# Performance work log

Measured on AMD Instinct MI355X. Metric: run time of the kernel, lower is better.

The kernel has to match this reference:

```python
import jax, jax.numpy as jnp
import numpy as np

N_NODES = 100000
N_EDGES = 1600000
N_GRAPHS = 512
NODE_DIM = 64   # len(node_indices)
GRAPH_DIM = 16  # len(graph_indices) == graph_channels
HIDDEN = 128
OUT = 8


def setup_inputs() -> dict:
    key = jax.random.key(0)
    ks = jax.random.split(key, 12)
    x = jax.random.normal(ks[0], (N_NODES, NODE_DIM + GRAPH_DIM), dtype=jnp.float32)
    edge_index = jax.random.randint(ks[1], (2, N_EDGES), 0, N_NODES, dtype=jnp.int64)
    batch = jnp.sort(jax.random.randint(ks[2], (N_NODES,), 0, N_GRAPHS, dtype=jnp.int64))
    def lin(k, fan_in, fan_out):
        lim = 1.0 / np.sqrt(fan_in)
        return jax.random.uniform(k, (fan_in, fan_out), jnp.float32, -lim, lim)
    return {
        "x": x, "edge_index": edge_index, "batch": batch,
        "W1": lin(ks[3], NODE_DIM, HIDDEN), "b1": jnp.zeros((HIDDEN,), jnp.float32),
        "W2": lin(ks[4], HIDDEN, HIDDEN),   "b2": jnp.zeros((HIDDEN,), jnp.float32),
        "Wm1": lin(ks[5], HIDDEN + GRAPH_DIM, HIDDEN), "bm1": jnp.zeros((HIDDEN,), jnp.float32),
        "Wm2": lin(ks[6], HIDDEN, OUT), "bm2": jnp.zeros((OUT,), jnp.float32),
    }


def _gcn_conv(h_in, src, dst, W, b):
    # PyG GCNConv: h = X W; out = D^{-1/2}(A+I)D^{-1/2} h + b, deg over A+I.
    h = h_in @ W                                        # [N, H]
    deg = jnp.zeros((N_NODES,), h.dtype).at[dst].add(1.0) + 1.0  # +1 self loop
    dinv = jax.lax.rsqrt(deg)                           # [N]
    norm = dinv[src] * dinv[dst]                        # [E]
    out = jnp.zeros_like(h).at[dst].add(norm[:, None] * h[src])
    out = out + (dinv * dinv)[:, None] * h              # self-loop term
    return out + b


def _mean_pool(v, batch):
    cnt = jax.ops.segment_sum(jnp.ones((v.shape[0],), v.dtype), batch, num_segments=N_GRAPHS)
    s = jax.ops.segment_sum(v, batch, num_segments=N_GRAPHS)
    return s / jnp.maximum(cnt, 1.0)[:, None]


def reference(x, edge_index, batch, W1, b1, W2, b2, Wm1, bm1, Wm2, bm2):
    src, dst = edge_index[0], edge_index[1]
    node_t = x[:, :NODE_DIM]                 # node_indices slice
    graph_t = _mean_pool(x[:, NODE_DIM:], batch)  # graph_indices slice, pooled [G, 16]
    h = _gcn_conv(node_t, src, dst, W1, b1)
    h = jax.nn.relu(h)                       # dropout is identity in eval mode
    h = _gcn_conv(h, src, dst, W2, b2)
    g = _mean_pool(h, batch)                 # [G, H]
    g = jnp.concatenate([g, graph_t], axis=1)
    g = jax.nn.relu(g @ Wm1 + bm1)
    return g @ Wm2 + bm2                     # [G, OUT]
```

## Files before the change

### kernel.cpp

```cpp
#include <hip/hip_runtime.h>
#include <hip/hip_bf16.h>

#define N_NODES 100000
#define N_EDGES 1600000
#define N_GRAPHS 512
#define NODE_DIM 64
#define GRAPH_DIM 16
#define HIDDEN 128
#define OUT_DIM 8

#define NBUCKETS 391
#define BIN_CAP 8192
#define EPB 4096

__device__ __forceinline__ float bflo(unsigned u) { return __uint_as_float(u << 16); }
__device__ __forceinline__ float bfhi(unsigned u) { return __uint_as_float(u & 0xffff0000u); }


__global__ __launch_bounds__(256) void k_binplace(const int* __restrict__ src,
                                                  const int* __restrict__ dst,
                                                  int* __restrict__ gcur,
                                                  unsigned* __restrict__ bin) {
    __shared__ int cnt[NBUCKETS];
    __shared__ int base[NBUCKETS];
    int t = threadIdx.x;
    for (int i = t; i < NBUCKETS; i += 256) cnt[i] = 0;
    __syncthreads();
    int e0 = blockIdx.x * EPB;
#pragma unroll
    for (int k = 0; k < EPB / 256; k++) {
        int e = e0 + k * 256 + t;
        if (e < N_EDGES) atomicAdd(&cnt[dst[e] >> 8], 1);
    }
    __syncthreads();
    for (int i = t; i < NBUCKETS; i += 256) {
        int c = cnt[i];
        base[i] = (c > 0) ? atomicAdd(&gcur[i], c) : 0;
        cnt[i] = 0;
    }
    __syncthreads();
#pragma unroll
    for (int k = 0; k < EPB / 256; k++) {
        int e = e0 + k * 256 + t;
        if (e < N_EDGES) {
            int d = dst[e];
            int b = d >> 8;
            int p = atomicAdd(&cnt[b], 1);
            bin[(size_t)b * BIN_CAP + base[b] + p] = ((unsigned)src[e] << 8) | (unsigned)(d & 255);
        }
    }
}


__global__ __launch_bounds__(256) void k_degBf(const int* __restrict__ gcur,
                                               const unsigned* __restrict__ bin,
                                               int* __restrict__ degcnt,
                                               float* __restrict__ dinv,
                                               int* __restrict__ bsum) {
    __shared__ int cnt[256];
    int b = blockIdx.x, t = threadIdx.x;
    cnt[t] = 0;
    __syncthreads();
    int n = gcur[b];
    const unsigned* seg = bin + (size_t)b * BIN_CAP;
    for (int i = t; i < n; i += 256) atomicAdd(&cnt[seg[i] & 255u], 1);
    __syncthreads();
    int c = cnt[t];
    int node = b * 256 + t;
    if (node < N_NODES) {
        degcnt[node] = c;
        dinv[node] = rsqrtf((float)c + 1.0f);
    }
    __syncthreads();
    for (int o = 128; o > 0; o >>= 1) {
        if (t < o) cnt[t] += cnt[t + o];
        __syncthreads();
    }
    if (t == 0) bsum[b] = cnt[0];
}


__global__ __launch_bounds__(512) void k_scanb(const int* __restrict__ bsum,
                                               int* __restrict__ bofs) {
    __shared__ int s[512];
    int t = threadIdx.x;
    int v = (t < NBUCKETS) ? bsum[t] : 0;
    s[t] = v;
    __syncthreads();
    for (int o = 1; o < 512; o <<= 1) {
        int u = (t >= o) ? s[t - o] : 0;
        __syncthreads();
        s[t] += u;
        __syncthreads();
    }
    if (t < NBUCKETS) bofs[t] = s[t] - v;
}


__global__ __launch_bounds__(256) void k_rowfill(const int* __restrict__ degcnt,
                                                 const int* __restrict__ bofs,
                                                 const int* __restrict__ gcur,
                                                 const unsigned* __restrict__ bin,
                                                 const float* __restrict__ dinv,
                                                 int* __restrict__ row_start,
                                                 int2* __restrict__ csre,
                                                 float* __restrict__ gt_sum) {
    __shared__ int sc[256];
    __shared__ int rsl[256];
    __shared__ int cnt[256];
    __shared__ float dl[256];
    int b = blockIdx.x, t = threadIdx.x;
    if (b < 32) gt_sum[b * 256 + t] = 0.0f;
    int node = b * 256 + t;
    int v = (node < N_NODES) ? degcnt[node] : 0;
    sc[t] = v;
    __syncthreads();
    for (int o = 1; o < 256; o <<= 1) {
        int u = (t >= o) ? sc[t - o] : 0;
        __syncthreads();
        sc[t] += u;
        __syncthreads();
    }
    int rs = bofs[b] + sc[t] - v;
    if (node < N_NODES) row_start[node] = rs;
    rsl[t] = rs;
    cnt[t] = 0;
    dl[t] = rsqrtf((float)v + 1.0f);
    __syncthreads();
    int n = gcur[b];
    const unsigned* seg = bin + (size_t)b * BIN_CAP;
    for (int i = t; i < n; i += 256) {
        unsigned e = seg[i];
        int dlidx = (int)(e & 255u);
        int s = (int)(e >> 8);
        int pos = rsl[dlidx] + atomicAdd(&cnt[dlidx], 1);
        csre[pos] = make_int2(s, __float_as_int(dinv[s] * dl[dlidx]));
    }
}


__global__ __launch_bounds__(256) void k_packstat(const float* __restrict__ x,
                                                  const int* __restrict__ batch,
                                                  ushort* __restrict__ xb,
                                                  float* __restrict__ gt_sum) {
    int t = threadIdx.x;
    int i0 = blockIdx.x * 64;
    for (int idx = t; idx < 64 * 32; idx += 256) {
        int node = i0 + (idx >> 5);
        if (node < N_NODES) {
            int c2 = idx & 31;
            float2 v = *(const float2*)&x[(size_t)node * 80 + c2 * 2];
            __hip_bfloat16 lo = __float2bfloat16(v.x);
            __hip_bfloat16 hi = __float2bfloat16(v.y);
            ushort2 pv = make_ushort2(*(ushort*)&lo, *(ushort*)&hi);
            ((ushort2*)xb)[(size_t)node * 32 + c2] = pv;
        }
    }
    int c = t & 15, sub = t >> 4;
    int iend = min(i0 + 64, N_NODES);
    float acc = 0.0f;
    int g = -1;
    for (int i = i0 + sub; i < iend; i += 16) {
        int bi = batch[i];
        if (bi != g) {
            if (g >= 0) atomicAdd(&gt_sum[g * GRAPH_DIM + c], acc);
            acc = 0.0f; g = bi;
        }
        acc += x[(size_t)i * 80 + NODE_DIM + c];
    }
    if (g >= 0) atomicAdd(&gt_sum[g * GRAPH_DIM + c], acc);
}


__global__ __launch_bounds__(256) void k_gather1(const int2* __restrict__ csre,
                                                 const int* __restrict__ row_start,
                                                 const float* __restrict__ dinv,
                                                 const unsigned* __restrict__ xb32,
                                                 float2* __restrict__ z2) {
    int w = threadIdx.x >> 6;
    int half = (threadIdx.x >> 5) & 1;
    int l = threadIdx.x & 31;
    int node = blockIdx.x * 8 + w * 2 + half;
    int rs = row_start[node];
    int re = (node == N_NODES - 1) ? N_EDGES : row_start[node + 1];
    float2 a0 = {0.f, 0.f}, a1 = {0.f, 0.f}, a2 = {0.f, 0.f}, a3 = {0.f, 0.f};
    int k = rs;
    for (; k + 4 <= re; k += 4) {
        int2 e0 = csre[k], e1 = csre[k + 1], e2 = csre[k + 2], e3 = csre[k + 3];
        unsigned u0 = xb32[(size_t)e0.x * 32 + l];
        unsigned u1 = xb32[(size_t)e1.x * 32 + l];
        unsigned u2 = xb32[(size_t)e2.x * 32 + l];
        unsigned u3 = xb32[(size_t)e3.x * 32 + l];
        float w0 = __int_as_float(e0.y), w1 = __int_as_float(e1.y);
        float w2 = __int_as_float(e2.y), w3 = __int_as_float(e3.y);
        a0.x += w0 * bflo(u0); a0.y += w0 * bfhi(u0);
        a1.x += w1 * bflo(u1); a1.y += w1 * bfhi(u1);
        a2.x += w2 * bflo(u2); a2.y += w2 * bfhi(u2);
        a3.x += w3 * bflo(u3); a3.y += w3 * bfhi(u3);
    }
    if (k + 2 <= re) {
        int2 e0 = csre[k], e1 = csre[k + 1];
        unsigned u0 = xb32[(size_t)e0.x * 32 + l];
        unsigned u1 = xb32[(size_t)e1.x * 32 + l];
        float w0 = __int_as_float(e0.y), w1 = __int_as_float(e1.y);
        a0.x += w0 * bflo(u0); a0.y += w0 * bfhi(u0);
        a1.x += w1 * bflo(u1); a1.y += w1 * bfhi(u1);
        k += 2;
    }
    if (k < re) {
        int2 e0 = csre[k];
        unsigned u0 = xb32[(size_t)e0.x * 32 + l];
        float w0 = __int_as_float(e0.y);
        a0.x += w0 * bflo(u0); a0.y += w0 * bfhi(u0);
    }
    float d = dinv[node];
    unsigned us = xb32[(size_t)node * 32 + l];
    float2 r;
    r.x = a0.x + a1.x + a2.x + a3.x + d * d * bflo(us);
    r.y = a0.y + a1.y + a2.y + a3.y + d * d * bfhi(us);
    z2[(size_t)node * 32 + l] = r;
}


__global__ __launch_bounds__(128) void k_gemm64(const float* __restrict__ A,
                                                const float* __restrict__ W,
                                                const float* __restrict__ bias,
                                                ushort* __restrict__ C, int nrows,
                                                float* __restrict__ gsum2) {
    const int TM = 8, K = 64;
    __shared__ float As[TM][K];
    if (blockIdx.x < 512) gsum2[blockIdx.x * 128 + threadIdx.x] = 0.0f;
    int row0 = blockIdx.x * TM;
    int j = threadIdx.x;
    for (int idx = threadIdx.x; idx < TM * K; idx += 128) {
        int m = idx / K, k = idx % K;
        int r = row0 + m;
        As[m][k] = (r < nrows) ? A[(size_t)r * K + k] : 0.0f;
    }
    __syncthreads();
    float acc[TM];
#pragma unroll
    for (int m = 0; m < TM; m++) acc[m] = 0.0f;
    for (int k = 0; k < K; k++) {
        float w = W[k * 128 + j];
#pragma unroll
        for (int m = 0; m < TM; m++) acc[m] += As[m][k] * w;
    }
    float b = bias[j];
#pragma unroll
    for (int m = 0; m < TM; m++) {
        int r = row0 + m;
        if (r < nrows) {
            float v = fmaxf(acc[m] + b, 0.0f);
            __hip_bfloat16 hv = __float2bfloat16(v);
            C[(size_t)r * 128 + j] = *(ushort*)&hv;
        }
    }
}


__global__ __launch_bounds__(256) void k_gather2(const int2* __restrict__ csre,
                                                 const int* __restrict__ row_start,
                                                 const float* __restrict__ dinv,
                                                 const uint2* __restrict__ h2,
                                                 const int* __restrict__ batch,
                                                 float* __restrict__ gsum2) {
    __shared__ float4 red[8][32];
    int w = threadIdx.x >> 6;
    int half = (threadIdx.x >> 5) & 1;
    int l = threadIdx.x & 31;
    int slot = w * 2 + half;
    int node = blockIdx.x * 8 + slot;
    int rs = row_start[node];
    int re = (node == N_NODES - 1) ? N_EDGES : row_start[node + 1];
    float4 a0 = {0,0,0,0}, a1 = {0,0,0,0}, a2 = {0,0,0,0}, a3 = {0,0,0,0};
#define FMA4(acc_, w_, u_) { acc_.x += (w_) * bflo((u_).x); acc_.y += (w_) * bfhi((u_).x); \
                             acc_.z += (w_) * bflo((u_).y); acc_.w += (w_) * bfhi((u_).y); }
    int k = rs;
    for (; k + 4 <= re; k += 4) {
        int2 e0 = csre[k], e1 = csre[k + 1], e2 = csre[k + 2], e3 = csre[k + 3];
        uint2 u0 = h2[(size_t)e0.x * 32 + l];
        uint2 u1 = h2[(size_t)e1.x * 32 + l];
        uint2 u2 = h2[(size_t)e2.x * 32 + l];
        uint2 u3 = h2[(size_t)e3.x * 32 + l];
        float w0 = __int_as_float(e0.y), w1 = __int_as_float(e1.y);
        float w2 = __int_as_float(e2.y), w3 = __int_as_float(e3.y);
        FMA4(a0, w0, u0); FMA4(a1, w1, u1); FMA4(a2, w2, u2); FMA4(a3, w3, u3);
    }
    if (k + 2 <= re) {
        int2 e0 = csre[k], e1 = csre[k + 1];
        uint2 u0 = h2[(size_t)e0.x * 32 + l];
        uint2 u1 = h2[(size_t)e1.x * 32 + l];
        float w0 = __int_as_float(e0.y), w1 = __int_as_float(e1.y);
        FMA4(a0, w0, u0); FMA4(a1, w1, u1);
        k += 2;
    }
    if (k < re) {
        int2 e0 = csre[k];
        uint2 u0 = h2[(size_t)e0.x * 32 + l];
        float w0 = __int_as_float(e0.y);
        FMA4(a0, w0, u0);
    }
#undef FMA4
    float d = dinv[node];
    float dd = d * d;
    uint2 us = h2[(size_t)node * 32 + l];
    float4 r;
    r.x = a0.x + a1.x + a2.x + a3.x + dd * bflo(us.x);
    r.y = a0.y + a1.y + a2.y + a3.y + dd * bfhi(us.x);
    r.z = a0.z + a1.z + a2.z + a3.z + dd * bflo(us.y);
    r.w = a0.w + a1.w + a2.w + a3.w + dd * bfhi(us.y);
    red[slot][l] = r;
    __syncthreads();
    int base8 = blockIdx.x * 8;
    int g0 = batch[base8];
    int g7 = batch[base8 + 7];
    if (g0 == g7) {
        if (threadIdx.x < 32) {
            float4 s = {0,0,0,0};
#pragma unroll
            for (int q = 0; q < 8; q++) {
                float4 v = red[q][threadIdx.x];
                s.x += v.x; s.y += v.y; s.z += v.z; s.w += v.w;
            }
            atomicAdd(&gsum2[g0 * 128 + threadIdx.x * 4 + 0], s.x);
            atomicAdd(&gsum2[g0 * 128 + threadIdx.x * 4 + 1], s.y);
            atomicAdd(&gsum2[g0 * 128 + threadIdx.x * 4 + 2], s.z);
            atomicAdd(&gsum2[g0 * 128 + threadIdx.x * 4 + 3], s.w);
        }
    } else {
        int g = batch[node];
        atomicAdd(&gsum2[g * 128 + l * 4 + 0], r.x);
        atomicAdd(&gsum2[g * 128 + l * 4 + 1], r.y);
        atomicAdd(&gsum2[g * 128 + l * 4 + 2], r.z);
        atomicAdd(&gsum2[g * 128 + l * 4 + 3], r.w);
    }
}


__global__ __launch_bounds__(128) void k_mlp(const float* __restrict__ gsum2,
                                             const float* __restrict__ gt_sum,
                                             const int* __restrict__ batch,
                                             const float* __restrict__ W2,
                                             const float* __restrict__ b2,
                                             const float* __restrict__ Wm1,
                                             const float* __restrict__ bm1,
                                             const float* __restrict__ Wm2,
                                             const float* __restrict__ bm2,
                                             float* __restrict__ out) {
    __shared__ float srow[HIDDEN];
    __shared__ float g144[HIDDEN + GRAPH_DIM];
    __shared__ float sm[HIDDEN];
    __shared__ int cnt_sh;
    int b = blockIdx.x;
    int j = threadIdx.x;
    float raw = gsum2[b * 128 + j];
    float gtraw = (j < GRAPH_DIM) ? gt_sum[b * GRAPH_DIM + j] : 0.0f;
    if (j == 0) {
        int lo = 0, hi = N_NODES;
        while (lo < hi) { int m = (lo + hi) >> 1; if (batch[m] < b) lo = m + 1; else hi = m; }
        int a = lo;
        lo = 0; hi = N_NODES;
        while (lo < hi) { int m = (lo + hi) >> 1; if (batch[m] < b + 1) lo = m + 1; else hi = m; }
        cnt_sh = lo - a;
    }
    __syncthreads();
    float inv = 1.0f / fmaxf((float)cnt_sh, 1.0f);
    srow[j] = raw * inv;
    if (j < GRAPH_DIM) g144[128 + j] = gtraw * inv;
    __syncthreads();
    float z = b2[j];
    for (int k = 0; k < 128; k++) z += srow[k] * W2[k * 128 + j];
    g144[j] = z;
    __syncthreads();
    float acc = bm1[j];
    for (int k = 0; k < HIDDEN + GRAPH_DIM; k++) acc += g144[k] * Wm1[k * 128 + j];
    sm[j] = fmaxf(acc, 0.0f);
    __syncthreads();
    if (j < OUT_DIM) {
        float o = bm2[j];
        for (int k = 0; k < 128; k++) o += sm[k] * Wm2[k * OUT_DIM + j];
        out[b * OUT_DIM + j] = o;
    }
}

extern "C" void kernel_launch(void* const* d_in, const int* in_sizes, int n_in,
                              void* d_out, int out_size, void* d_ws, size_t ws_size,
                              hipStream_t stream) {
    const float* x    = (const float*)d_in[0];
    const int*   edge = (const int*)d_in[1];
    const int*   src  = edge;
    const int*   dst  = edge + N_EDGES;
    const int*   batch= (const int*)d_in[2];
    const float* W1   = (const float*)d_in[3];
    const float* b1   = (const float*)d_in[4];
    const float* W2   = (const float*)d_in[5];
    const float* b2   = (const float*)d_in[6];
    const float* Wm1  = (const float*)d_in[7];
    const float* bm1  = (const float*)d_in[8];
    const float* Wm2  = (const float*)d_in[9];
    const float* bm2  = (const float*)d_in[10];
    float* out = (float*)d_out;

    char* ws = (char*)d_ws;
    char* p = ws;
    unsigned* bin   = (unsigned*)p;  p += (size_t)NBUCKETS * BIN_CAP * 4;
    int2*  csre     = (int2*)p;      p += (size_t)N_EDGES * 8;
    float* A        = (float*)p;     p += (size_t)N_NODES * 64 * 4;
    ushort* h1b     = (ushort*)p;    p += (size_t)N_NODES * 128 * 2;
    ushort* xb      = (ushort*)p;    p += (size_t)N_NODES * 64 * 2;
    int*   degcnt   = (int*)p;       p += (size_t)NBUCKETS * 256 * 4;
    int*   row_start= (int*)p;       p += (size_t)N_NODES * 4;
    float* dinv     = (float*)p;     p += (size_t)N_NODES * 4;
    int*   gcur     = (int*)p;       p += (size_t)NBUCKETS * 4;
    int*   bsum     = (int*)p;       p += 512 * 4;
    int*   bofs     = (int*)p;       p += 512 * 4;
    float* gt_sum   = (float*)p;     p += (size_t)N_GRAPHS * GRAPH_DIM * 4;
    float* gsum2    = (float*)p;     p += (size_t)N_GRAPHS * 128 * 4;

    hipMemsetAsync(gcur, 0, (size_t)NBUCKETS * 4, stream);

    k_binplace<<<(N_EDGES + EPB - 1) / EPB, 256, 0, stream>>>(src, dst, gcur, bin);
    k_degBf<<<NBUCKETS, 256, 0, stream>>>(gcur, bin, degcnt, dinv, bsum);
    k_scanb<<<1, 512, 0, stream>>>(bsum, bofs);
    k_rowfill<<<NBUCKETS, 256, 0, stream>>>(degcnt, bofs, gcur, bin, dinv, row_start, csre, gt_sum);

    k_packstat<<<(N_NODES + 63) / 64, 256, 0, stream>>>(x, batch, xb, gt_sum);

    k_gather1<<<N_NODES / 8, 256, 0, stream>>>(csre, row_start, dinv, (const unsigned*)xb, (float2*)A);
    k_gemm64<<<(N_NODES + 7) / 8, 128, 0, stream>>>(A, W1, b1, h1b, N_NODES, gsum2);

    k_gather2<<<N_NODES / 8, 256, 0, stream>>>(csre, row_start, dinv,
                                               (const uint2*)h1b, batch, gsum2);

    k_mlp<<<N_GRAPHS, 128, 0, stream>>>(gsum2, gt_sum, batch, W2, b2, Wm1, bm1, Wm2, bm2, out);
}
```

Before: 258.1 us.

## Fuse layer-1 gather with the 64x128 GEMM and use a full wave per node

Merges the first aggregation kernel with the dense W1 transform, so aggregated rows stay in shared memory and are never written to or read back from the fp32 intermediate buffer. Both gather kernels now give each node a full 64-lane wave, with the two halves taking alternate edges and combining via a cross-half shuffle, and blocks grow to 512 threads. This removes a launch and an intermediate round trip and raises per-node memory parallelism. In exchange there is more shuffle and select work per edge, and the fused GEMM runs on only 8 rows per block, each thread re-reading W1 from global memory.

```diff
diff --git a/kernel.cpp b/kernel.cpp
--- a/kernel.cpp
+++ b/kernel.cpp
@@ -172,168 +172,175 @@
 }
 
 
-__global__ __launch_bounds__(256) void k_gather1(const int2* __restrict__ csre,
-                                                 const int* __restrict__ row_start,
-                                                 const float* __restrict__ dinv,
-                                                 const unsigned* __restrict__ xb32,
-                                                 float2* __restrict__ z2) {
-    int w = threadIdx.x >> 6;
-    int half = (threadIdx.x >> 5) & 1;
-    int l = threadIdx.x & 31;
-    int node = blockIdx.x * 8 + w * 2 + half;
+__global__ __launch_bounds__(512) void k_conv1(const int2* __restrict__ csre,
+                                               const int* __restrict__ row_start,
+                                               const float* __restrict__ dinv,
+                                               const unsigned* __restrict__ xb32,
+                                               const float* __restrict__ W,
+                                               const float* __restrict__ bias,
+                                               ushort* __restrict__ C,
+                                               float* __restrict__ gsum2) {
+    __shared__ float zs[8][64];
+    int t = threadIdx.x;
+    if (blockIdx.x < 128) gsum2[blockIdx.x * 512 + t] = 0.0f;
+    int wv = t >> 6;
+    int lane = t & 63;
+    int half = lane >> 5;
+    int l5 = lane & 31;
+    int node = blockIdx.x * 8 + wv;
     int rs = row_start[node];
     int re = (node == N_NODES - 1) ? N_EDGES : row_start[node + 1];
-    float2 a0 = {0.f, 0.f}, a1 = {0.f, 0.f}, a2 = {0.f, 0.f}, a3 = {0.f, 0.f};
+    float2 a0 = {0.f,0.f}, a1 = {0.f,0.f}, a2 = {0.f,0.f}, a3 = {0.f,0.f};
     int k = rs;
-    for (; k + 4 <= re; k += 4) {
-        int2 e0 = csre[k], e1 = csre[k + 1], e2 = csre[k + 2], e3 = csre[k + 3];
-        unsigned u0 = xb32[(size_t)e0.x * 32 + l];
-        unsigned u1 = xb32[(size_t)e1.x * 32 + l];
-        unsigned u2 = xb32[(size_t)e2.x * 32 + l];
-        unsigned u3 = xb32[(size_t)e3.x * 32 + l];
-        float w0 = __int_as_float(e0.y), w1 = __int_as_float(e1.y);
-        float w2 = __int_as_float(e2.y), w3 = __int_as_float(e3.y);
+    for (; k + 8 <= re; k += 8) {
+        int2 e0 = csre[k],     e1 = csre[k + 1], e2 = csre[k + 2], e3 = csre[k + 3];
+        int2 e4 = csre[k + 4], e5 = csre[k + 5], e6 = csre[k + 6], e7 = csre[k + 7];
+        int   r0 = half ? e1.x : e0.x;  float w0 = __int_as_float(half ? e1.y : e0.y);
+        int   r1 = half ? e3.x : e2.x;  float w1 = __int_as_float(half ? e3.y : e2.y);
+        int   r2 = half ? e5.x : e4.x;  float w2 = __int_as_float(half ? e5.y : e4.y);
+        int   r3 = half ? e7.x : e6.x;  float w3 = __int_as_float(half ? e7.y : e6.y);
+        unsigned u0 = xb32[(size_t)r0 * 32 + l5];
+        unsigned u1 = xb32[(size_t)r1 * 32 + l5];
+        unsigned u2 = xb32[(size_t)r2 * 32 + l5];
+        unsigned u3 = xb32[(size_t)r3 * 32 + l5];
         a0.x += w0 * bflo(u0); a0.y += w0 * bfhi(u0);
         a1.x += w1 * bflo(u1); a1.y += w1 * bfhi(u1);
         a2.x += w2 * bflo(u2); a2.y += w2 * bfhi(u2);
         a3.x += w3 * bflo(u3); a3.y += w3 * bfhi(u3);
     }
-    if (k + 2 <= re) {
+    for (; k + 2 <= re; k += 2) {
         int2 e0 = csre[k], e1 = csre[k + 1];
-        unsigned u0 = xb32[(size_t)e0.x * 32 + l];
-        unsigned u1 = xb32[(size_t)e1.x * 32 + l];
-        float w0 = __int_as_float(e0.y), w1 = __int_as_float(e1.y);
+        int r0 = half ? e1.x : e0.x;  float w0 = __int_as_float(half ? e1.y : e0.y);
+        unsigned u0 = xb32[(size_t)r0 * 32 + l5];
         a0.x += w0 * bflo(u0); a0.y += w0 * bfhi(u0);
-        a1.x += w1 * bflo(u1); a1.y += w1 * bfhi(u1);
-        k += 2;
     }
     if (k < re) {
         int2 e0 = csre[k];
-        unsigned u0 = xb32[(size_t)e0.x * 32 + l];
-        float w0 = __int_as_float(e0.y);
+        float w0 = half ? 0.0f : __int_as_float(e0.y);
+        unsigned u0 = xb32[(size_t)e0.x * 32 + l5];
         a0.x += w0 * bflo(u0); a0.y += w0 * bfhi(u0);
     }
-    float d = dinv[node];
-    unsigned us = xb32[(size_t)node * 32 + l];
-    float2 r;
-    r.x = a0.x + a1.x + a2.x + a3.x + d * d * bflo(us);
-    r.y = a0.y + a1.y + a2.y + a3.y + d * d * bfhi(us);
-    z2[(size_t)node * 32 + l] = r;
-}
-
-
-__global__ __launch_bounds__(128) void k_gemm64(const float* __restrict__ A,
-                                                const float* __restrict__ W,
-                                                const float* __restrict__ bias,
-                                                ushort* __restrict__ C, int nrows,
-                                                float* __restrict__ gsum2) {
-    const int TM = 8, K = 64;
-    __shared__ float As[TM][K];
-    if (blockIdx.x < 512) gsum2[blockIdx.x * 128 + threadIdx.x] = 0.0f;
-    int row0 = blockIdx.x * TM;
-    int j = threadIdx.x;
-    for (int idx = threadIdx.x; idx < TM * K; idx += 128) {
-        int m = idx / K, k = idx % K;
-        int r = row0 + m;
-        As[m][k] = (r < nrows) ? A[(size_t)r * K + k] : 0.0f;
-    }
-    __syncthreads();
-    float acc[TM];
-#pragma unroll
-    for (int m = 0; m < TM; m++) acc[m] = 0.0f;
-    for (int k = 0; k < K; k++) {
-        float w = W[k * 128 + j];
-#pragma unroll
-        for (int m = 0; m < TM; m++) acc[m] += As[m][k] * w;
-    }
-    float b = bias[j];
-#pragma unroll
-    for (int m = 0; m < TM; m++) {
-        int r = row0 + m;
-        if (r < nrows) {
-            float v = fmaxf(acc[m] + b, 0.0f);
-            __hip_bfloat16 hv = __float2bfloat16(v);
-            C[(size_t)r * 128 + j] = *(ushort*)&hv;
+    float sx = a0.x + a1.x + a2.x + a3.x;
+    float sy = a0.y + a1.y + a2.y + a3.y;
+    sx += __shfl_xor(sx, 32);
+    sy += __shfl_xor(sy, 32);
+    if (half == 0) {
+        float d = dinv[node];
+        float dd = d * d;
+        unsigned us = xb32[(size_t)node * 32 + l5];
+        zs[wv][2 * l5]     = sx + dd * bflo(us);
+        zs[wv][2 * l5 + 1] = sy + dd * bfhi(us);
+    }
+    __syncthreads();
+    {
+        int j = t & 127;
+        int g = t >> 7;
+        float acc0 = 0.f, acc1 = 0.f;
+        for (int kk = 0; kk < 64; kk++) {
+            float wk = W[kk * 128 + j];
+            acc0 += zs[2 * g][kk] * wk;
+            acc1 += zs[2 * g + 1][kk] * wk;
         }
-    }
-}
-
-
-__global__ __launch_bounds__(256) void k_gather2(const int2* __restrict__ csre,
+        float b = bias[j];
+        size_t row0 = (size_t)blockIdx.x * 8 + 2 * g;
+        float v0 = fmaxf(acc0 + b, 0.0f);
+        float v1 = fmaxf(acc1 + b, 0.0f);
+        __hip_bfloat16 h0 = __float2bfloat16(v0);
+        __hip_bfloat16 h1 = __float2bfloat16(v1);
+        C[row0 * 128 + j]       = *(ushort*)&h0;
+        C[(row0 + 1) * 128 + j] = *(ushort*)&h1;
+    }
+}
+
+
+__global__ __launch_bounds__(512) void k_gather2(const int2* __restrict__ csre,
                                                  const int* __restrict__ row_start,
                                                  const float* __restrict__ dinv,
                                                  const uint2* __restrict__ h2,
                                                  const int* __restrict__ batch,
                                                  float* __restrict__ gsum2) {
     __shared__ float4 red[8][32];
-    int w = threadIdx.x >> 6;
-    int half = (threadIdx.x >> 5) & 1;
-    int l = threadIdx.x & 31;
-    int slot = w * 2 + half;
-    int node = blockIdx.x * 8 + slot;
+    int t = threadIdx.x;
+    int wv = t >> 6;
+    int lane = t & 63;
+    int half = lane >> 5;
+    int l5 = lane & 31;
+    int node = blockIdx.x * 8 + wv;
     int rs = row_start[node];
     int re = (node == N_NODES - 1) ? N_EDGES : row_start[node + 1];
     float4 a0 = {0,0,0,0}, a1 = {0,0,0,0}, a2 = {0,0,0,0}, a3 = {0,0,0,0};
 #define FMA4(acc_, w_, u_) { acc_.x += (w_) * bflo((u_).x); acc_.y += (w_) * bfhi((u_).x); \
                              acc_.z += (w_) * bflo((u_).y); acc_.w += (w_) * bfhi((u_).y); }
     int k = rs;
-    for (; k + 4 <= re; k += 4) {
-        int2 e0 = csre[k], e1 = csre[k + 1], e2 = csre[k + 2], e3 = csre[k + 3];
-        uint2 u0 = h2[(size_t)e0.x * 32 + l];
-        uint2 u1 = h2[(size_t)e1.x * 32 + l];
-        uint2 u2 = h2[(size_t)e2.x * 32 + l];
-        uint2 u3 = h2[(size_t)e3.x * 32 + l];
-        float w0 = __int_as_float(e0.y), w1 = __int_as_float(e1.y);
-        float w2 = __int_as_float(e2.y), w3 = __int_as_float(e3.y);
+    for (; k + 8 <= re; k += 8) {
+        int2 e0 = csre[k],     e1 = csre[k + 1], e2 = csre[k + 2], e3 = csre[k + 3];
+        int2 e4 = csre[k + 4], e5 = csre[k + 5], e6 = csre[k + 6], e7 = csre[k + 7];
+        int   r0 = half ? e1.x : e0.x;  float w0 = __int_as_float(half ? e1.y : e0.y);
+        int   r1 = half ? e3.x : e2.x;  float w1 = __int_as_float(half ? e3.y : e2.y);
+        int   r2 = half ? e5.x : e4.x;  float w2 = __int_as_float(half ? e5.y : e4.y);
+        int   r3 = half ? e7.x : e6.x;  float w3 = __int_as_float(half ? e7.y : e6.y);
+        uint2 u0 = h2[(size_t)r0 * 32 + l5];
+        uint2 u1 = h2[(size_t)r1 * 32 + l5];
+        uint2 u2 = h2[(size_t)r2 * 32 + l5];
+        uint2 u3 = h2[(size_t)r3 * 32 + l5];
         FMA4(a0, w0, u0); FMA4(a1, w1, u1); FMA4(a2, w2, u2); FMA4(a3, w3, u3);
     }
-    if (k + 2 <= re) {
+    for (; k + 2 <= re; k += 2) {
         int2 e0 = csre[k], e1 = csre[k + 1];
-        uint2 u0 = h2[(size_t)e0.x * 32 + l];
-        uint2 u1 = h2[(size_t)e1.x * 32 + l];
-        float w0 = __int_as_float(e0.y), w1 = __int_as_float(e1.y);
-        FMA4(a0, w0, u0); FMA4(a1, w1, u1);
-        k += 2;
+        int r0 = half ? e1.x : e0.x;  float w0 = __int_as_float(half ? e1.y : e0.y);
+        uint2 u0 = h2[(size_t)r0 * 32 + l5];
+        FMA4(a0, w0, u0);
     }
     if (k < re) {
         int2 e0 = csre[k];
-        uint2 u0 = h2[(size_t)e0.x * 32 + l];
-        float w0 = __int_as_float(e0.y);
+        float w0 = half ? 0.0f : __int_as_float(e0.y);
+        uint2 u0 = h2[(size_t)e0.x * 32 + l5];
         FMA4(a0, w0, u0);
     }
 #undef FMA4
-    float d = dinv[node];
-    float dd = d * d;
-    uint2 us = h2[(size_t)node * 32 + l];
+    float4 s;
+    s.x = a0.x + a1.x + a2.x + a3.x;
+    s.y = a0.y + a1.y + a2.y + a3.y;
+    s.z = a0.z + a1.z + a2.z + a3.z;
+    s.w = a0.w + a1.w + a2.w + a3.w;
+    s.x += __shfl_xor(s.x, 32);
+    s.y += __shfl_xor(s.y, 32);
+    s.z += __shfl_xor(s.z, 32);
+    s.w += __shfl_xor(s.w, 32);
     float4 r;
-    r.x = a0.x + a1.x + a2.x + a3.x + dd * bflo(us.x);
-    r.y = a0.y + a1.y + a2.y + a3.y + dd * bfhi(us.x);
-    r.z = a0.z + a1.z + a2.z + a3.z + dd * bflo(us.y);
-    r.w = a0.w + a1.w + a2.w + a3.w + dd * bfhi(us.y);
-    red[slot][l] = r;
+    if (half == 0) {
+        float d = dinv[node];
+        float dd = d * d;
+        uint2 us = h2[(size_t)node * 32 + l5];
+        r.x = s.x + dd * bflo(us.x);
+        r.y = s.y + dd * bfhi(us.x);
+        r.z = s.z + dd * bflo(us.y);
+        r.w = s.w + dd * bfhi(us.y);
+        red[wv][l5] = r;
+    }
     __syncthreads();
     int base8 = blockIdx.x * 8;
     int g0 = batch[base8];
     int g7 = batch[base8 + 7];
     if (g0 == g7) {
-        if (threadIdx.x < 32) {
-            float4 s = {0,0,0,0};
+        if (t < 32) {
+            float4 acc = {0,0,0,0};
 #pragma unroll
             for (int q = 0; q < 8; q++) {
-                float4 v = red[q][threadIdx.x];
-                s.x += v.x; s.y += v.y; s.z += v.z; s.w += v.w;
+                float4 v = red[q][t];
+                acc.x += v.x; acc.y += v.y; acc.z += v.z; acc.w += v.w;
             }
-            atomicAdd(&gsum2[g0 * 128 + threadIdx.x * 4 + 0], s.x);
-            atomicAdd(&gsum2[g0 * 128 + threadIdx.x * 4 + 1], s.y);
-            atomicAdd(&gsum2[g0 * 128 + threadIdx.x * 4 + 2], s.z);
-            atomicAdd(&gsum2[g0 * 128 + threadIdx.x * 4 + 3], s.w);
+            atomicAdd(&gsum2[g0 * 128 + t * 4 + 0], acc.x);
+            atomicAdd(&gsum2[g0 * 128 + t * 4 + 1], acc.y);
+            atomicAdd(&gsum2[g0 * 128 + t * 4 + 2], acc.z);
+            atomicAdd(&gsum2[g0 * 128 + t * 4 + 3], acc.w);
         }
-    } else {
+    } else if (half == 0) {
         int g = batch[node];
-        atomicAdd(&gsum2[g * 128 + l * 4 + 0], r.x);
-        atomicAdd(&gsum2[g * 128 + l * 4 + 1], r.y);
-        atomicAdd(&gsum2[g * 128 + l * 4 + 2], r.z);
-        atomicAdd(&gsum2[g * 128 + l * 4 + 3], r.w);
+        atomicAdd(&gsum2[g * 128 + l5 * 4 + 0], r.x);
+        atomicAdd(&gsum2[g * 128 + l5 * 4 + 1], r.y);
+        atomicAdd(&gsum2[g * 128 + l5 * 4 + 2], r.z);
+        atomicAdd(&gsum2[g * 128 + l5 * 4 + 3], r.w);
     }
 }
 
@@ -406,7 +413,6 @@
     char* p = ws;
     unsigned* bin   = (unsigned*)p;  p += (size_t)NBUCKETS * BIN_CAP * 4;
     int2*  csre     = (int2*)p;      p += (size_t)N_EDGES * 8;
-    float* A        = (float*)p;     p += (size_t)N_NODES * 64 * 4;
     ushort* h1b     = (ushort*)p;    p += (size_t)N_NODES * 128 * 2;
     ushort* xb      = (ushort*)p;    p += (size_t)N_NODES * 64 * 2;
     int*   degcnt   = (int*)p;       p += (size_t)NBUCKETS * 256 * 4;
@@ -427,10 +433,10 @@
 
     k_packstat<<<(N_NODES + 63) / 64, 256, 0, stream>>>(x, batch, xb, gt_sum);
 
-    k_gather1<<<N_NODES / 8, 256, 0, stream>>>(csre, row_start, dinv, (const unsigned*)xb, (float2*)A);
-    k_gemm64<<<(N_NODES + 7) / 8, 128, 0, stream>>>(A, W1, b1, h1b, N_NODES, gsum2);
-
-    k_gather2<<<N_NODES / 8, 256, 0, stream>>>(csre, row_start, dinv,
+    k_conv1<<<N_NODES / 8, 512, 0, stream>>>(csre, row_start, dinv, (const unsigned*)xb,
+                                             W1, b1, h1b, gsum2);
+
+    k_gather2<<<N_NODES / 8, 512, 0, stream>>>(csre, row_start, dinv,
                                                (const uint2*)h1b, batch, gsum2);
 
     k_mlp<<<N_GRAPHS, 128, 0, stream>>>(gsum2, gt_sum, batch, W2, b2, Wm1, bm1, Wm2, bm2, out);
```

Result: slower. 300.9 us (+16.6%).
